# Performance work log

Hardware: AMD Instinct MI355X
Metric: run time of the kernel (lower is better)

Reference implementation:

```python
import jax, jax.numpy as jnp
import numpy as np

B, D, H, O = 8192, 512, 16384, 1000

def _row_normalize(w):
    return w / jnp.linalg.norm(w, axis=1, keepdims=True)

def setup_inputs() -> dict:
    key = jax.random.key(0)
    k0, k1, k2, k3 = jax.random.split(key, 4)
    x = jax.random.normal(k0, (B, D), dtype=jnp.float32)
    kohonen_weights = _row_normalize(jax.random.normal(k1, (H, D), dtype=jnp.float32))
    G_fwd = _row_normalize(jax.random.normal(k2, (O, H), dtype=jnp.float32))
    G_rev = _row_normalize(jax.random.normal(k3, (D, H), dtype=jnp.float32))
    return {"x": x, "kohonen_weights": kohonen_weights, "G_fwd": G_fwd, "G_rev": G_rev}

def reference(x, kohonen_weights, G_fwd, G_rev):
    # torch.cdist(x, W): Euclidean distances, shape (B, H).
    x2 = jnp.sum(x * x, axis=1, keepdims=True)          # (B, 1)
    w2 = jnp.sum(kohonen_weights * kohonen_weights, axis=1)  # (H,)
    d2 = x2 - 2.0 * (x @ kohonen_weights.T) + w2[None, :]    # (B, H)
    distances = jnp.sqrt(jnp.maximum(d2, 0.0))
    winners = jnp.argmin(distances, axis=1)              # (B,)
    # one_hot @ G_fwd.T == gather of G_fwd columns (same math, no dense GEMM)
    output = G_fwd.T[winners]                            # (B, O)
    recos = G_rev.T[winners]                             # (B, D)
    return (output, recos, winners)
```

## Files before the change

### kernel.cpp

```cpp
#include <hip/hip_runtime.h>
#include <stdint.h>

constexpr int kB = 8192;
constexpr int kD = 512;
constexpr int kH = 16384;
constexpr int kO = 1000;
constexpr int kNB64 = kH / 64;
constexpr float kMargin = 0.055f;

typedef _Float16 half8v __attribute__((ext_vector_type(8)));
typedef _Float16 half4v __attribute__((ext_vector_type(4)));
typedef float float4v __attribute__((ext_vector_type(4)));

#define VMW(n) asm volatile("s_waitcnt vmcnt(" #n ")" ::: "memory")

constexpr size_t OFF_XH  = 0;
constexpr size_t OFF_WH  = OFF_XH + (size_t)kB * kD * 2;
constexpr size_t OFF_W2  = OFF_WH + (size_t)kH * kD * 2;
constexpr size_t OFF_BT  = OFF_W2 + 65536;
constexpr size_t OFF_GFT = OFF_BT + (size_t)kB * kNB64 * 8;
constexpr size_t OFF_GRT = OFF_GFT + (size_t)kH * kO * 4;
constexpr size_t WS_NEED = OFF_GRT + (size_t)kH * kD * 4;

__device__ inline unsigned mono32(float s) {
    unsigned u = __float_as_uint(s);
    return u ^ ((u & 0x80000000u) ? 0xFFFFFFFFu : 0x80000000u);
}
__device__ inline float dq32(unsigned key) {
    unsigned u = key & 0xFFFFFFC0u;
    u ^= (u & 0x80000000u) ? 0x80000000u : 0xFFFFFFFFu;
    return __uint_as_float(u);
}
__device__ inline unsigned long long packkey(float s, int h) {
    return ((unsigned long long)mono32(s) << 32) | (unsigned)h;
}
__device__ inline unsigned long long u64min(unsigned long long a, unsigned long long b) {
    return a < b ? a : b;
}

template <typename T>
__device__ inline void gload_lds16(const T* g, T* l) {
    __builtin_amdgcn_global_load_lds(
        (const __attribute__((address_space(1))) uint32_t*)g,
        (__attribute__((address_space(3))) uint32_t*)l, 16, 0, 0);
}

__global__ __launch_bounds__(256) void prep_kernel(const float* __restrict__ x,
                                                   const float* __restrict__ W,
                                                   _Float16* __restrict__ xh,
                                                   _Float16* __restrict__ wh,
                                                   float* __restrict__ w2) {
    if (blockIdx.x < 2048) {
        size_t i = (size_t)blockIdx.x * 256 + threadIdx.x;
        const float4* s4 = reinterpret_cast<const float4*>(x);
        float4 a = s4[i * 2], b = s4[i * 2 + 1];
        half8v h = {(_Float16)a.x, (_Float16)a.y, (_Float16)a.z, (_Float16)a.w,
                    (_Float16)b.x, (_Float16)b.y, (_Float16)b.z, (_Float16)b.w};
        *reinterpret_cast<half8v*>(xh + i * 8) = h;
    } else {
        int bx = blockIdx.x - 2048;
        int lane = threadIdx.x & 63;
        int wv   = threadIdx.x >> 6;
        int row  = bx * 4 + wv;
        const float4* Wr = reinterpret_cast<const float4*>(W + (size_t)row * kD);
        float s = 0.f;
#pragma unroll
        for (int i = 0; i < 2; ++i) {
            float4 v = Wr[lane + i * 64];
            s += v.x * v.x + v.y * v.y + v.z * v.z + v.w * v.w;
            half4v h = {(_Float16)v.x, (_Float16)v.y, (_Float16)v.z, (_Float16)v.w};
            *reinterpret_cast<half4v*>(wh + (size_t)row * kD + i * 256 + lane * 4) = h;
        }
#pragma unroll
        for (int off = 32; off; off >>= 1) s += __shfl_xor(s, off, 64);
        if (lane == 0) w2[row] = s;
    }
}

__global__ __launch_bounds__(256) void transpose2_kernel(const float* __restrict__ Gf,
                                                         float* __restrict__ GfT,
                                                         const float* __restrict__ Gr,
                                                         float* __restrict__ GrT,
                                                         int useTf, int useTr) {
    const float* src; float* dst; int R, r0;
    if (blockIdx.y < 32) {
        if (!useTf) return;
        src = Gf; dst = GfT; R = kO; r0 = blockIdx.y * 32;
    } else {
        if (!useTr) return;
        src = Gr; dst = GrT; R = kD; r0 = (blockIdx.y - 32) * 32;
    }
    const int C = kH;
    __shared__ float s[32][33];
    const int tx = threadIdx.x & 31;
    const int ty = threadIdx.x >> 5;
    const int c0 = blockIdx.x * 32;
#pragma unroll
    for (int i = 0; i < 4; ++i) {
        int r = r0 + ty + i * 8;
        if (r < R) s[ty + i * 8][tx] = src[(size_t)r * C + c0 + tx];
    }
    __syncthreads();
#pragma unroll
    for (int i = 0; i < 4; ++i) {
        int c = c0 + ty + i * 8;
        if (r0 + tx < R) dst[(size_t)c * R + r0 + tx] = s[tx][ty + i * 8];
    }
}

__global__ __launch_bounds__(512, 2) void gemm_argmin_mfma(
    const _Float16* __restrict__ xh, const _Float16* __restrict__ wh,
    const float* __restrict__ w2, uint2* __restrict__ blocktop)
{
    __shared__ __align__(16) _Float16 sm[65536];

    const int tid  = threadIdx.x;
    const int lane = tid & 63;
    const int wv   = tid >> 6;
    const int wr   = wv >> 2;
    const int wc   = wv & 3;

    int bid = blockIdx.x;
    const int mb  = bid >> 6;
    const int hb  = (bid & 7) * 8 + ((bid >> 3) & 7);
    const int bm0 = mb * 256, hn0 = hb * 256;

    float4v acc[8][4];
#pragma unroll
    for (int i = 0; i < 8; ++i)
#pragma unroll
        for (int j = 0; j < 4; ++j) acc[i][j] = (float4v){0.f, 0.f, 0.f, 0.f};

    auto STAGEH = [&](int h) {
        const int T2 = h >> 2, jp = h & 3;
        const int kk = jp >> 1, isB = jp & 1;
        const int kt = T2 * 64 + kk * 32;
        _Float16* dst0 = &sm[(((T2 & 1) << 2) | jp) * 8192 + wv * 512];
#pragma unroll
        for (int l = 0; l < 2; ++l) {
            const int idx = l * 512 + tid;
            const int r = idx >> 2, c = idx & 3;
            const int sc = c ^ ((r >> 1) & 3);
            const _Float16* src =
                (isB ? wh + (size_t)(hn0 + r) * kD : xh + (size_t)(bm0 + r) * kD)
                + kt + sc * 8;
            gload_lds16(src, dst0 + l * 4096);
        }
    };

    auto HALF = [&](int buf, int kk, int hstage) {
        const int fbase = buf * 32768 + kk * 16384;
        half8v bfr[4], afr[8];
#pragma unroll
        for (int jn = 0; jn < 4; ++jn) {
            const int r = wc * 64 + jn * 16 + (lane & 15);
            const int cs = (lane >> 4) ^ ((r >> 1) & 3);
            bfr[jn] = *reinterpret_cast<const half8v*>(&sm[fbase + 8192 + r * 32 + cs * 8]);
        }
#pragma unroll
        for (int im = 0; im < 8; ++im) {
            const int r = wr * 128 + im * 16 + (lane & 15);
            const int cs = (lane >> 4) ^ ((r >> 1) & 3);
            afr[im] = *reinterpret_cast<const half8v*>(&sm[fbase + r * 32 + cs * 8]);
        }
        if (hstage >= 0) {
            STAGEH(hstage);
            STAGEH(hstage + 1);
        }
        asm volatile("s_waitcnt lgkmcnt(0)" ::: "memory");
        __builtin_amdgcn_sched_barrier(0);
        __builtin_amdgcn_s_setprio(1);
#pragma unroll
        for (int im = 0; im < 8; ++im)
#pragma unroll
            for (int jn = 0; jn < 4; ++jn)
                acc[im][jn] =
                    __builtin_amdgcn_mfma_f32_16x16x32_f16(afr[im], bfr[jn],
                                                           acc[im][jn], 0, 0, 0);
        __builtin_amdgcn_s_setprio(0);
    };

    STAGEH(0); STAGEH(1); STAGEH(2); STAGEH(3);
    VMW(0);
    __builtin_amdgcn_s_barrier();

#pragma unroll
    for (int T = 0; T < 8; ++T) {
        const int buf = T & 1;
        const int hs = (T < 7) ? 4 * (T + 1) : -2;
        HALF(buf, 0, hs);
        HALF(buf, 1, hs >= 0 ? hs + 2 : -2);
        if (T < 7) {
            VMW(0);
            __builtin_amdgcn_s_barrier();
        }
    }

    float w2v[4];
#pragma unroll
    for (int j = 0; j < 4; ++j) w2v[j] = w2[hn0 + wc * 64 + j * 16 + (lane & 15)];

#pragma unroll
    for (int i = 0; i < 8; ++i) {
#pragma unroll
        for (int r = 0; r < 4; ++r) {
            unsigned k1 = 0xFFFFFFFFu, k2 = 0xFFFFFFFFu;
#pragma unroll
            for (int j = 0; j < 4; ++j) {
                float s = fmaf(-2.f, acc[i][j][r], w2v[j]);
                unsigned key = (mono32(s) & 0xFFFFFFC0u)
                             | (unsigned)(j * 16 + (lane & 15));
                if (key < k1) { k2 = k1; k1 = key; }
                else if (key < k2) { k2 = key; }
            }
#pragma unroll
            for (int m = 1; m < 16; m <<= 1) {
                unsigned o1 = (unsigned)__shfl_xor((int)k1, m, 64);
                unsigned o2 = (unsigned)__shfl_xor((int)k2, m, 64);
                unsigned n1 = min(k1, o1);
                unsigned mx = max(k1, o1);
                k2 = min(min(k2, o2), mx);
                k1 = n1;
            }
            if ((lane & 15) == 0) {
                int rl = wr * 128 + i * 16 + (lane >> 4) * 4 + r;
                blocktop[(size_t)(bm0 + rl) * kNB64 + hb * 4 + wc] =
                    (uint2){k1, k2};
            }
        }
    }
}

__global__ __launch_bounds__(256) void finish_kernel(
    const float* __restrict__ x, const float* __restrict__ W,
    const float* __restrict__ w2, const uint2* __restrict__ blocktop,
    const float* __restrict__ Gf, const float* __restrict__ Gr,
    const float* __restrict__ GfT, const float* __restrict__ GrT,
    int useTf, int useTr, float* __restrict__ out)
{
    const int tid = threadIdx.x;
    const int b = blockIdx.x;
    __shared__ float xs[kD];
    __shared__ unsigned long long red[256];
    __shared__ unsigned long long sv1, sv2;
    __shared__ int clist[kNB64];
    __shared__ int ccount;

    if (tid < 128)
        reinterpret_cast<float4*>(xs)[tid] =
            reinterpret_cast<const float4*>(x + (size_t)b * kD)[tid];
    if (tid == 0) ccount = 0;

    uint2 t12 = blocktop[(size_t)b * kNB64 + tid];

    red[tid] = ((unsigned long long)t12.x << 8) | (unsigned)tid;
    __syncthreads();
    for (int s = 128; s > 0; s >>= 1) {
        if (tid < s) red[tid] = u64min(red[tid], red[tid + s]);
        __syncthreads();
    }
    if (tid == 0) sv1 = red[0];
    __syncthreads();
    const unsigned long long v1k = sv1;
    const int b1hb = (int)(v1k & 0xFFu);
    const unsigned v1key = (unsigned)(v1k >> 8);
    const float v1s = dq32(v1key);
    const int v1h = b1hb * 64 + (int)(v1key & 63u);

    red[tid] = ((unsigned long long)((tid == b1hb) ? t12.y : t12.x) << 8) | (unsigned)tid;
    __syncthreads();
    for (int s = 128; s > 0; s >>= 1) {
        if (tid < s) red[tid] = u64min(red[tid], red[tid + s]);
        __syncthreads();
    }
    if (tid == 0) sv2 = red[0];
    __syncthreads();
    const float v2s = dq32((unsigned)(sv2 >> 8));

    int idx;
    if (v2s - v1s > kMargin) {
        idx = v1h;
    } else {
        if (dq32(t12.x) <= v1s + kMargin) {
            int p = atomicAdd(&ccount, 1);
            clist[p] = tid;
        }
        __syncthreads();
        const int nc = ccount;
        const int wvf = tid >> 6, lnf = tid & 63;
        unsigned long long bestk = ~0ull;
        for (int c = wvf; c < nc; c += 4) {
            int h = clist[c] * 64 + lnf;
            const float4* wr = reinterpret_cast<const float4*>(W + (size_t)h * kD);
            float dot = 0.f;
            for (int k = 0; k < kD / 4; ++k) {
                float4 wvv = wr[k];
                dot = fmaf(xs[k * 4 + 0], wvv.x, dot);
                dot = fmaf(xs[k * 4 + 1], wvv.y, dot);
                dot = fmaf(xs[k * 4 + 2], wvv.z, dot);
                dot = fmaf(xs[k * 4 + 3], wvv.w, dot);
            }
            float s = fmaf(-2.f, dot, w2[h]);
            bestk = u64min(bestk, packkey(s, h));
        }
        red[tid] = bestk;
        __syncthreads();
        for (int s = 128; s > 0; s >>= 1) {
            if (tid < s) red[tid] = u64min(red[tid], red[tid + s]);
            __syncthreads();
        }
        idx = (int)(unsigned)(red[0] & 0xFFFFFFFFu);
    }

    float* out0 = out;
    float* out1 = out + (size_t)kB * kO;
    float* outw = out + (size_t)kB * (kO + kD);
    if (useTf) {
        const float4* gfr = reinterpret_cast<const float4*>(GfT + (size_t)idx * kO);
        float4* o0 = reinterpret_cast<float4*>(out0 + (size_t)b * kO);
        for (int o = tid; o < kO / 4; o += 256) o0[o] = gfr[o];
    } else {
        for (int o = tid; o < kO; o += 256)
            out0[(size_t)b * kO + o] = Gf[(size_t)o * kH + idx];
    }
    if (useTr) {
        const float4* grr = reinterpret_cast<const float4*>(GrT + (size_t)idx * kD);
        float4* o1 = reinterpret_cast<float4*>(out1 + (size_t)b * kD);
        if (tid < kD / 4) o1[tid] = grr[tid];
    } else {
        for (int d = tid; d < kD; d += 256)
            out1[(size_t)b * kD + d] = Gr[(size_t)d * kH + idx];
    }
    if (tid == 0) outw[b] = (float)idx;
}

extern "C" void kernel_launch(void* const* d_in, const int* in_sizes, int n_in,
                              void* d_out, int out_size, void* d_ws, size_t ws_size,
                              hipStream_t stream) {
    const float* x  = (const float*)d_in[0];
    const float* W  = (const float*)d_in[1];
    const float* Gf = (const float*)d_in[2];
    const float* Gr = (const float*)d_in[3];
    float* out = (float*)d_out;

    char* ws = (char*)d_ws;
    _Float16* xh = (_Float16*)(ws + OFF_XH);
    _Float16* wh = (_Float16*)(ws + OFF_WH);
    float* w2 = (float*)(ws + OFF_W2);
    uint2* blocktop = (uint2*)(ws + OFF_BT);
    float* GfT = (float*)(ws + OFF_GFT);
    float* GrT = (float*)(ws + OFF_GRT);
    const int useTf = (ws_size >= OFF_GRT) ? 1 : 0;
    const int useTr = (ws_size >= WS_NEED) ? 1 : 0;

    hipLaunchKernelGGL(prep_kernel, dim3(2048 + 4096), dim3(256), 0, stream,
                       x, W, xh, wh, w2);
    if (useTf || useTr)
        hipLaunchKernelGGL(transpose2_kernel, dim3(kH / 32, 48), dim3(256), 0, stream,
                           Gf, GfT, Gr, GrT, useTf, useTr);
    hipLaunchKernelGGL(gemm_argmin_mfma, dim3(2048), dim3(512), 0, stream,
                       xh, wh, w2, blocktop);
    hipLaunchKernelGGL(finish_kernel, dim3(kB), dim3(256), 0, stream,
                       x, W, w2, blocktop, Gf, Gr, GfT, GrT, useTf, useTr, out);
}
```

Measured before the change: 315.3 us.

## Shrink LDS staging to K=32 double buffer with barrier per step

Cuts the shared-memory tile from two 64-wide K stages to two 32-wide K stages and runs 16 pipeline steps with a barrier after each, instead of 8 steps with two MFMA halves per barrier. LDS use per block halves (128KB to 64KB), which may let more blocks or waves stay resident under the launch bounds. The cost is twice as many barriers and vmcnt waits, plus less prefetch distance to hide global load latency.

```diff
diff --git a/kernel.cpp b/kernel.cpp
--- a/kernel.cpp
+++ b/kernel.cpp
@@ -112,7 +112,7 @@
     const _Float16* __restrict__ xh, const _Float16* __restrict__ wh,
     const float* __restrict__ w2, uint2* __restrict__ blocktop)
 {
-    __shared__ __align__(16) _Float16 sm[65536];
+    __shared__ __align__(16) _Float16 sm[32768];
 
     const int tid  = threadIdx.x;
     const int lane = tid & 63;
@@ -131,25 +131,23 @@
 #pragma unroll
         for (int j = 0; j < 4; ++j) acc[i][j] = (float4v){0.f, 0.f, 0.f, 0.f};
 
-    auto STAGEH = [&](int h) {
-        const int T2 = h >> 2, jp = h & 3;
-        const int kk = jp >> 1, isB = jp & 1;
-        const int kt = T2 * 64 + kk * 32;
-        _Float16* dst0 = &sm[(((T2 & 1) << 2) | jp) * 8192 + wv * 512];
+    auto STAGE = [&](int t) {
+        const int kt = t * 32;
+        _Float16* base = &sm[(t & 1) * 16384];
 #pragma unroll
         for (int l = 0; l < 2; ++l) {
             const int idx = l * 512 + tid;
             const int r = idx >> 2, c = idx & 3;
             const int sc = c ^ ((r >> 1) & 3);
-            const _Float16* src =
-                (isB ? wh + (size_t)(hn0 + r) * kD : xh + (size_t)(bm0 + r) * kD)
-                + kt + sc * 8;
-            gload_lds16(src, dst0 + l * 4096);
+            gload_lds16(xh + (size_t)(bm0 + r) * kD + kt + sc * 8,
+                        base + (wv * 512 + l * 4096));
+            gload_lds16(wh + (size_t)(hn0 + r) * kD + kt + sc * 8,
+                        base + 8192 + (wv * 512 + l * 4096));
         }
     };
 
-    auto HALF = [&](int buf, int kk, int hstage) {
-        const int fbase = buf * 32768 + kk * 16384;
+    auto STEP = [&](int t, bool doStage) {
+        const int fbase = (t & 1) * 16384;
         half8v bfr[4], afr[8];
 #pragma unroll
         for (int jn = 0; jn < 4; ++jn) {
@@ -163,10 +161,7 @@
             const int cs = (lane >> 4) ^ ((r >> 1) & 3);
             afr[im] = *reinterpret_cast<const half8v*>(&sm[fbase + r * 32 + cs * 8]);
         }
-        if (hstage >= 0) {
-            STAGEH(hstage);
-            STAGEH(hstage + 1);
-        }
+        if (doStage) STAGE(t + 1);
         asm volatile("s_waitcnt lgkmcnt(0)" ::: "memory");
         __builtin_amdgcn_sched_barrier(0);
         __builtin_amdgcn_s_setprio(1);
@@ -180,17 +175,14 @@
         __builtin_amdgcn_s_setprio(0);
     };
 
-    STAGEH(0); STAGEH(1); STAGEH(2); STAGEH(3);
+    STAGE(0);
     VMW(0);
     __builtin_amdgcn_s_barrier();
 
 #pragma unroll
-    for (int T = 0; T < 8; ++T) {
-        const int buf = T & 1;
-        const int hs = (T < 7) ? 4 * (T + 1) : -2;
-        HALF(buf, 0, hs);
-        HALF(buf, 1, hs >= 0 ? hs + 2 : -2);
-        if (T < 7) {
+    for (int t = 0; t < 16; ++t) {
+        STEP(t, t < 15);
+        if (t < 15) {
             VMW(0);
             __builtin_amdgcn_s_barrier();
         }
```

Result: no change. 318.3 us (+0.9%).
